# Optimization experiments

Measured on AMD Instinct MI355X. Metric: run time of the kernel, lower is better.

The kernel has to match this reference:

```python
import jax, jax.numpy as jnp
import numpy as np

NUM_EXPERTS = 8
TOP_K = 2
B, L, H = 4, 4096, 1024


def setup_inputs() -> dict:
    key = jax.random.key(0)
    ks = jax.random.split(key, 5)
    s = 1.0 / np.sqrt(H)
    return {
        "hidden_states": jax.random.normal(ks[0], (B, L, H), dtype=jnp.float32),
        "gate_w": jax.random.normal(ks[1], (H, NUM_EXPERTS), dtype=jnp.float32) * s,
        "w1": jax.random.normal(ks[2], (NUM_EXPERTS, H, 2 * H), dtype=jnp.float32) * s,
        "b1": jnp.zeros((NUM_EXPERTS, 2 * H), dtype=jnp.float32),
        "w2": jax.random.normal(ks[3], (NUM_EXPERTS, 2 * H, H), dtype=jnp.float32) * (1.0 / np.sqrt(2 * H)),
        "b2": jnp.zeros((NUM_EXPERTS, H), dtype=jnp.float32),
    }


def reference(hidden_states, gate_w, w1, b1, w2, b2):
    b, l, h = hidden_states.shape
    flat = hidden_states.reshape(-1, h)                      # [T, H]
    router_logits = flat @ gate_w                            # [T, E]
    probs = jax.nn.softmax(router_logits, axis=-1)
    weights, indices = jax.lax.top_k(probs, TOP_K)           # [T, K]
    weights = weights / jnp.sum(weights, axis=-1, keepdims=True)
    # combine[t, e] = sum_k weights[t, k] * 1{indices[t, k] == e}
    onehot = jax.nn.one_hot(indices, NUM_EXPERTS, dtype=flat.dtype)  # [T, K, E]
    combine = jnp.einsum('tk,tke->te', weights, onehot)      # [T, E]
    out = jnp.zeros_like(flat)
    for e in range(NUM_EXPERTS):  # fixed small expert loop; dense-compute, sparse-combine
        hdn = jax.nn.relu(flat @ w1[e] + b1[e])              # [T, 2H]
        y = hdn @ w2[e] + b2[e]                              # [T, H]
        out = out + combine[:, e:e + 1] * y
    return out.reshape(b, l, h)
```

## Files before the change

### kernel.cpp

```cpp
#include <hip/hip_runtime.h>
#include <hip/hip_bf16.h>
#include <stdint.h>

#define T_TOK 16384
#define HD    1024
#define HD2   2048
#define NE    8
#define ROWS  (2*T_TOK)
#define MAXT  264
#define RTOK  32

#define M_NT    256
#define M_OFFS  272
#define M_TILES 288

typedef __bf16 bf16x8 __attribute__((ext_vector_type(8)));
typedef float f32x4 __attribute__((ext_vector_type(4)));

#define GLD16(g, l) __builtin_amdgcn_global_load_lds( \
    (const __attribute__((address_space(1))) void*)(g), \
    (__attribute__((address_space(3))) void*)(l), 16, 0, 0)

__device__ inline unsigned short f2bf(float f) {
    unsigned int u = __float_as_uint(f);
    unsigned int r = (u + 0x7fffu + ((u >> 16) & 1u)) >> 16;
    return (unsigned short)r;
}

__global__ __launch_bounds__(256) void cvt_wT(const float* __restrict__ w,
                                              unsigned short* __restrict__ wt,
                                              int K, int N) {
    __shared__ float t[32][33];
    int e = blockIdx.z;
    int n0 = blockIdx.x * 32, k0 = blockIdx.y * 32;
    int r = threadIdx.x >> 3;
    int c4 = (threadIdx.x & 7) * 4;
    const float* src = w + ((size_t)e * K + k0 + r) * N + n0 + c4;
    float4 v = *(const float4*)src;
    t[r][c4] = v.x; t[r][c4+1] = v.y; t[r][c4+2] = v.z; t[r][c4+3] = v.w;
    __syncthreads();
    int cc = threadIdx.x & 7;
    ushort4 o;
    o.x = f2bf(t[cc*4+0][r]); o.y = f2bf(t[cc*4+1][r]);
    o.z = f2bf(t[cc*4+2][r]); o.w = f2bf(t[cc*4+3][r]);
    *(ushort4*)(wt + ((size_t)e * N + n0 + r) * K + k0 + cc*4) = o;
}

__global__ __launch_bounds__(256) void router_k(const float* __restrict__ x,
        const float* __restrict__ gw, int* __restrict__ meta,
        int* __restrict__ tok_e, int* __restrict__ tok_slot, float* __restrict__ tok_w,
        unsigned short* __restrict__ xb) {
    __shared__ float g[NE * HD];
    __shared__ int   le[RTOK * 2];
    __shared__ float lw[RTOK * 2];
    __shared__ int   lslot[RTOK * 2];
    __shared__ int   lcnt[NE];
    __shared__ int   lbase[NE];
    for (int i = threadIdx.x; i < NE * HD; i += 256) {
        int k = i >> 3, e = i & 7;
        g[e * HD + k] = gw[i];
    }
    if (threadIdx.x < NE) lcnt[threadIdx.x] = 0;
    __syncthreads();

    int wave = threadIdx.x >> 6, lane = threadIdx.x & 63;
    int t0 = blockIdx.x * RTOK;
    for (int i = 0; i < RTOK / 4; i++) {
        int tt = wave * (RTOK / 4) + i;
        int t = t0 + tt;
        const float4* xr = (const float4*)(x + (size_t)t * HD);
        float acc[NE];
#pragma unroll
        for (int e = 0; e < NE; e++) acc[e] = 0.f;
#pragma unroll
        for (int j = 0; j < HD / 256; j++) {
            float4 xv = xr[lane + 64 * j];
            ushort4 o4;
            o4.x = f2bf(xv.x); o4.y = f2bf(xv.y);
            o4.z = f2bf(xv.z); o4.w = f2bf(xv.w);
            *(ushort4*)(xb + (size_t)t * HD + (lane + 64 * j) * 4) = o4;
#pragma unroll
            for (int e = 0; e < NE; e++) {
                float4 gv = *(const float4*)&g[e * HD + (lane + 64 * j) * 4];
                acc[e] += xv.x * gv.x + xv.y * gv.y + xv.z * gv.z + xv.w * gv.w;
            }
        }
#pragma unroll
        for (int e = 0; e < NE; e++) {
            float v = acc[e];
#pragma unroll
            for (int off = 32; off > 0; off >>= 1) v += __shfl_down(v, off, 64);
            acc[e] = v;
        }
        if (lane == 0) {
            int e1 = 0; float l1 = acc[0];
#pragma unroll
            for (int e = 1; e < NE; e++) if (acc[e] > l1) { l1 = acc[e]; e1 = e; }
            int e2 = -1; float l2 = -3.0e38f;
#pragma unroll
            for (int e = 0; e < NE; e++) if (e != e1 && acc[e] > l2) { l2 = acc[e]; e2 = e; }
            float w1 = 1.f / (1.f + expf(l2 - l1));
            le[tt * 2] = e1;     le[tt * 2 + 1] = e2;
            lw[tt * 2] = w1;     lw[tt * 2 + 1] = 1.f - w1;
        }
    }
    __syncthreads();
    if (threadIdx.x < RTOK * 2)
        lslot[threadIdx.x] = atomicAdd(&lcnt[le[threadIdx.x]], 1);
    __syncthreads();
    if (threadIdx.x < NE)
        lbase[threadIdx.x] = atomicAdd(&meta[threadIdx.x * 32], lcnt[threadIdx.x]);
    __syncthreads();
    if (threadIdx.x < RTOK * 2) {
        int gi = t0 * 2 + threadIdx.x;
        int e = le[threadIdx.x];
        tok_e[gi]    = e;
        tok_slot[gi] = lbase[e] + lslot[threadIdx.x];
        tok_w[gi]    = lw[threadIdx.x];
    }
}

__global__ __launch_bounds__(64) void offsets_k(int* __restrict__ meta) {
    int lane = threadIdx.x;
    int cl = (lane < NE) ? meta[lane * 32] : 0;
    int cnt[NE], offs[NE], tbase[NE];
    int o = 0, tb = 0;
#pragma unroll
    for (int e = 0; e < NE; e++) {
        cnt[e] = __shfl(cl, e, 64);
        offs[e] = o;  o += cnt[e];
        tbase[e] = tb; tb += (cnt[e] + 127) >> 7;
    }
    int nt = tb;
    if (lane == 0) meta[M_NT] = nt;
    if (lane < NE) meta[M_OFFS + lane] = offs[lane];
    for (int i = lane; i < nt; i += 64) {
        int e = 0;
#pragma unroll
        for (int k = 1; k < NE; k++) if (i >= tbase[k]) e = k;
        int m = i - tbase[e];
        int r0 = offs[e] + m * 128;
        int re = offs[e] + cnt[e];
        if (r0 + 128 < re) re = r0 + 128;
        meta[M_TILES + i] = e;
        meta[M_TILES + MAXT + i] = r0;
        meta[M_TILES + 2 * MAXT + i] = re;
    }
}

__global__ __launch_bounds__(256) void scatter_k(const int* __restrict__ meta,
        const int* __restrict__ tok_e, const int* __restrict__ tok_slot,
        const float* __restrict__ tok_w, int* __restrict__ rows_tok,
        float* __restrict__ rows_w) {
    int i = blockIdx.x * 256 + threadIdx.x;
    const int* offs = meta + M_OFFS;
    int e = tok_e[i];
    int r = offs[e] + tok_slot[i];
    rows_tok[r] = i >> 1;
    rows_w[r] = tok_w[i];
}


#define ISSUE(KK, NT_) do { \
    int kk_ = (KK) < (NT_) ? (KK) : (NT_) - 1; \
    int bb_ = ((KK) & 1) * 4096; \
    GLD16(pa0 + kk_ * 32, &As[bb_ + (w * 64) * 8]); \
    GLD16(pa1 + kk_ * 32, &As[bb_ + (256 + w * 64) * 8]); \
    GLD16(pb0 + kk_ * 32, &Bs[bb_ + (w * 64) * 8]); \
    GLD16(pb1 + kk_ * 32, &Bs[bb_ + (256 + w * 64) * 8]); } while (0)
#define SB0()   __builtin_amdgcn_sched_barrier(0)
#define VMW4()  do { asm volatile("s_waitcnt vmcnt(4)" ::: "memory"); SB0(); } while (0)
#define VMW0()  do { asm volatile("s_waitcnt vmcnt(0)" ::: "memory"); SB0(); } while (0)
#define BAR()   do { __builtin_amdgcn_s_barrier(); SB0(); } while (0)
#define PRIO(P) __builtin_amdgcn_s_setprio(P)

#define KSTEP(RB) do { \
    bf16x8 af[4], bfr[4]; \
    _Pragma("unroll") \
    for (int in_ = 0; in_ < 4; in_++) { \
        int row_ = wn * 64 + in_ * 16 + rl; \
        int ph_ = q ^ ((row_ >> 1) & 3); \
        bfr[in_] = *(const bf16x8*)&Bs[(RB) + row_ * 32 + ph_ * 8]; \
    } \
    _Pragma("unroll") \
    for (int im_ = 0; im_ < 4; im_++) { \
        int row_ = wm * 64 + im_ * 16 + rl; \
        int ph_ = q ^ ((row_ >> 1) & 3); \
        af[im_] = *(const bf16x8*)&As[(RB) + row_ * 32 + ph_ * 8]; \
    } \
    _Pragma("unroll") \
    for (int im_ = 0; im_ < 4; im_++) \
    _Pragma("unroll") \
    for (int in_ = 0; in_ < 4; in_++) \
        acc[im_][in_] = __builtin_amdgcn_mfma_f32_16x16x32_bf16( \
            af[im_], bfr[in_], acc[im_][in_], 0, 0, 0); } while (0)

__global__ __launch_bounds__(256, 4) void gemm1_k(
    const unsigned short* __restrict__ Xbf,
    const unsigned short* __restrict__ W1T,
    const float* __restrict__ b1,
    const int* __restrict__ meta,
    const int* __restrict__ rows_tok,
    unsigned short* __restrict__ hdn)
{
    __shared__ unsigned short As[2 * 4096];
    __shared__ unsigned short Bs[2 * 4096];
    int nt = meta[M_NT];
    int mt = blockIdx.y;
    if (mt >= nt) return;
    int e    = meta[M_TILES + mt];
    int r0   = meta[M_TILES + MAXT + mt];
    int rend = meta[M_TILES + 2 * MAXT + mt];
    int n0 = blockIdx.x * 128;

    int tid = threadIdx.x, w = tid >> 6, lane = tid & 63;
    int wm = w & 1, wn = w >> 1;
    int rl = lane & 15, q = lane >> 4;

    const unsigned short *pa0, *pa1, *pb0, *pb1;
    {
        int gg = tid, row = gg >> 2, lc = (gg & 3) ^ ((row >> 1) & 3);
        int grow = r0 + row; grow = grow < ROWS - 1 ? grow : ROWS - 1;
        pa0 = Xbf + (size_t)rows_tok[grow] * HD + lc * 8;
        pb0 = W1T + ((size_t)e * HD2 + n0 + row) * HD + lc * 8;
        gg = 256 + tid; row = gg >> 2; lc = (gg & 3) ^ ((row >> 1) & 3);
        grow = r0 + row; grow = grow < ROWS - 1 ? grow : ROWS - 1;
        pa1 = Xbf + (size_t)rows_tok[grow] * HD + lc * 8;
        pb1 = W1T + ((size_t)e * HD2 + n0 + row) * HD + lc * 8;
    }

    f32x4 acc[4][4];
#pragma unroll
    for (int a = 0; a < 4; a++)
#pragma unroll
    for (int b = 0; b < 4; b++)
        acc[a][b] = (f32x4){0.f, 0.f, 0.f, 0.f};

    ISSUE(0, HD / 32);

#pragma unroll 2
    for (int kt = 0; kt < HD / 32; kt++) {
        ISSUE(kt + 1, HD / 32);
        SB0();
        VMW4();
        BAR();
        PRIO(1);
        KSTEP((kt & 1) * 4096);
        PRIO(0);
        BAR();
    }
    VMW0();

    const float* b1e = b1 + (size_t)e * HD2;
#pragma unroll
    for (int in = 0; in < 4; in++) {
        int col = n0 + wn * 64 + in * 16 + rl;
        float bias = b1e[col];
#pragma unroll
        for (int im = 0; im < 4; im++) {
            int rb2 = r0 + wm * 64 + im * 16 + q * 4;
#pragma unroll
            for (int j = 0; j < 4; j++) {
                int r = rb2 + j;
                if (r < rend) {
                    float v = acc[im][in][j] + bias;
                    v = v > 0.f ? v : 0.f;
                    hdn[(size_t)r * HD2 + col] = f2bf(v);
                }
            }
        }
    }
}

__global__ __launch_bounds__(256, 4) void gemm2_k(
    const unsigned short* __restrict__ hdn,
    const unsigned short* __restrict__ W2T,
    const float* __restrict__ b2,
    const int* __restrict__ meta,
    const int* __restrict__ rows_tok,
    const float* __restrict__ rows_w,
    float* __restrict__ out)
{
    __shared__ unsigned short As[2 * 4096];
    __shared__ unsigned short Bs[2 * 4096];
    int nt = meta[M_NT];
    int mt = blockIdx.y;
    if (mt >= nt) return;
    int e    = meta[M_TILES + mt];
    int r0   = meta[M_TILES + MAXT + mt];
    int rend = meta[M_TILES + 2 * MAXT + mt];
    int n0 = blockIdx.x * 128;

    int tid = threadIdx.x, w = tid >> 6, lane = tid & 63;
    int wm = w & 1, wn = w >> 1;
    int rl = lane & 15, q = lane >> 4;

    const unsigned short *pa0, *pa1, *pb0, *pb1;
    {
        int gg = tid, row = gg >> 2, lc = (gg & 3) ^ ((row >> 1) & 3);
        int grow = r0 + row; grow = grow < ROWS - 1 ? grow : ROWS - 1;
        pa0 = hdn + (size_t)grow * HD2 + lc * 8;
        pb0 = W2T + ((size_t)e * HD + n0 + row) * HD2 + lc * 8;
        gg = 256 + tid; row = gg >> 2; lc = (gg & 3) ^ ((row >> 1) & 3);
        grow = r0 + row; grow = grow < ROWS - 1 ? grow : ROWS - 1;
        pa1 = hdn + (size_t)grow * HD2 + lc * 8;
        pb1 = W2T + ((size_t)e * HD + n0 + row) * HD2 + lc * 8;
    }

    f32x4 acc[4][4];
#pragma unroll
    for (int a = 0; a < 4; a++)
#pragma unroll
    for (int b = 0; b < 4; b++)
        acc[a][b] = (f32x4){0.f, 0.f, 0.f, 0.f};

    ISSUE(0, HD2 / 32);

#pragma unroll 2
    for (int kt = 0; kt < HD2 / 32; kt++) {
        ISSUE(kt + 1, HD2 / 32);
        SB0();
        VMW4();
        BAR();
        PRIO(1);
        KSTEP((kt & 1) * 4096);
        PRIO(0);
        BAR();
    }
    VMW0();

    const float* b2e = b2 + (size_t)e * HD;
    float bias[4];
#pragma unroll
    for (int in = 0; in < 4; in++)
        bias[in] = b2e[n0 + wn * 64 + in * 16 + rl];
#pragma unroll
    for (int im = 0; im < 4; im++) {
        int rb2 = r0 + wm * 64 + im * 16 + q * 4;
#pragma unroll
        for (int j = 0; j < 4; j++) {
            int r = rb2 + j;
            if (r < rend) {
                int tok = rows_tok[r];
                float wt = rows_w[r];
                float* op = out + (size_t)tok * HD + n0 + wn * 64;
#pragma unroll
                for (int in = 0; in < 4; in++) {
                    float v = (acc[im][in][j] + bias[in]) * wt;
                    atomicAdd(op + in * 16 + rl, v);
                }
            }
        }
    }
}

extern "C" void kernel_launch(void* const* d_in, const int* in_sizes, int n_in,
                              void* d_out, int out_size, void* d_ws, size_t ws_size,
                              hipStream_t stream) {
    const float* x  = (const float*)d_in[0];
    const float* gw = (const float*)d_in[1];
    const float* w1 = (const float*)d_in[2];
    const float* b1 = (const float*)d_in[3];
    const float* w2 = (const float*)d_in[4];
    const float* b2 = (const float*)d_in[5];
    float* out = (float*)d_out;

    uint8_t* ws = (uint8_t*)d_ws;
    unsigned short* Xbf = (unsigned short*)(ws);
    unsigned short* W1T = (unsigned short*)(ws + 33554432ull);
    unsigned short* W2T = (unsigned short*)(ws + 67108864ull);
    unsigned short* HDN = (unsigned short*)(ws + 100663296ull);
    int*   meta     = (int*)(ws + 234881024ull);
    int*   tok_e    = meta + 2048;
    int*   tok_slot = tok_e + ROWS;
    float* tok_w    = (float*)(tok_slot + ROWS);
    int*   rows_tok = (int*)(tok_w + ROWS);
    float* rows_w   = (float*)(rows_tok + ROWS);

    hipMemsetAsync(meta, 0, 1024, stream);
    hipMemsetAsync(d_out, 0, (size_t)out_size * sizeof(float), stream);

    cvt_wT<<<dim3(HD2 / 32, HD / 32, NE), 256, 0, stream>>>(w1, W1T, HD, HD2);
    cvt_wT<<<dim3(HD / 32, HD2 / 32, NE), 256, 0, stream>>>(w2, W2T, HD2, HD);
    router_k<<<T_TOK / RTOK, 256, 0, stream>>>(x, gw, meta, tok_e, tok_slot, tok_w, Xbf);
    offsets_k<<<1, 64, 0, stream>>>(meta);
    scatter_k<<<ROWS / 256, 256, 0, stream>>>(meta, tok_e, tok_slot, tok_w, rows_tok, rows_w);
    gemm1_k<<<dim3(HD2 / 128, MAXT), 256, 0, stream>>>(Xbf, W1T, b1, meta, rows_tok, HDN);
    gemm2_k<<<dim3(HD / 128, MAXT), 256, 0, stream>>>(HDN, W2T, b2, meta, rows_tok, rows_w, out);
}
```

Measured before the change: 730.8 us.

## Merge weight conversions, drop offsets kernel, stage gemm1 epilogue through LDS

```diff
diff --git a/kernel.cpp b/kernel.cpp
--- a/kernel.cpp
+++ b/kernel.cpp
@@ -10,12 +10,10 @@
 #define MAXT  264
 #define RTOK  32
 
-#define M_NT    256
-#define M_OFFS  272
-#define M_TILES 288
 
 typedef __bf16 bf16x8 __attribute__((ext_vector_type(8)));
 typedef float f32x4 __attribute__((ext_vector_type(4)));
+typedef unsigned short u16x8 __attribute__((ext_vector_type(8)));
 
 #define GLD16(g, l) __builtin_amdgcn_global_load_lds( \
     (const __attribute__((address_space(1))) void*)(g), \
@@ -27,12 +25,35 @@
     return (unsigned short)r;
 }
 
-__global__ __launch_bounds__(256) void cvt_wT(const float* __restrict__ w,
-                                              unsigned short* __restrict__ wt,
-                                              int K, int N) {
+__device__ inline void tile_locate(const int* __restrict__ meta, int mt,
+                                   int* e_out, int* r0_out, int* re_out) {
+    int o = 0, tb = 0, se = -1, sr0 = 0, sre = 0;
+#pragma unroll
+    for (int k = 0; k < NE; k++) {
+        int c = meta[k * 32];
+        int t = (c + 127) >> 7;
+        if (mt >= tb && mt < tb + t) {
+            se = k;
+            sr0 = o + (mt - tb) * 128;
+            int re = o + c;
+            sre = (sr0 + 128 < re) ? sr0 + 128 : re;
+        }
+        o += c; tb += t;
+    }
+    *e_out = se; *r0_out = sr0; *re_out = sre;
+}
+
+__global__ __launch_bounds__(256) void cvt_all(const float* __restrict__ w1,
+                                               const float* __restrict__ w2,
+                                               unsigned short* __restrict__ W1T,
+                                               unsigned short* __restrict__ W2T) {
     __shared__ float t[32][33];
-    int e = blockIdx.z;
+    int z = blockIdx.z;
+    const float* w; unsigned short* wt; int K, N, e;
+    if (z < 8) { w = w1; wt = W1T; K = HD;  N = HD2; e = z; }
+    else       { w = w2; wt = W2T; K = HD2; N = HD;  e = z - 8; }
     int n0 = blockIdx.x * 32, k0 = blockIdx.y * 32;
+    if (n0 >= N || k0 >= K) return;
     int r = threadIdx.x >> 3;
     int c4 = (threadIdx.x & 7) * 4;
     const float* src = w + ((size_t)e * K + k0 + r) * N + n0 + c4;
@@ -120,42 +141,19 @@
     }
 }
 
-__global__ __launch_bounds__(64) void offsets_k(int* __restrict__ meta) {
-    int lane = threadIdx.x;
-    int cl = (lane < NE) ? meta[lane * 32] : 0;
-    int cnt[NE], offs[NE], tbase[NE];
-    int o = 0, tb = 0;
-#pragma unroll
-    for (int e = 0; e < NE; e++) {
-        cnt[e] = __shfl(cl, e, 64);
-        offs[e] = o;  o += cnt[e];
-        tbase[e] = tb; tb += (cnt[e] + 127) >> 7;
-    }
-    int nt = tb;
-    if (lane == 0) meta[M_NT] = nt;
-    if (lane < NE) meta[M_OFFS + lane] = offs[lane];
-    for (int i = lane; i < nt; i += 64) {
-        int e = 0;
-#pragma unroll
-        for (int k = 1; k < NE; k++) if (i >= tbase[k]) e = k;
-        int m = i - tbase[e];
-        int r0 = offs[e] + m * 128;
-        int re = offs[e] + cnt[e];
-        if (r0 + 128 < re) re = r0 + 128;
-        meta[M_TILES + i] = e;
-        meta[M_TILES + MAXT + i] = r0;
-        meta[M_TILES + 2 * MAXT + i] = re;
-    }
-}
-
 __global__ __launch_bounds__(256) void scatter_k(const int* __restrict__ meta,
         const int* __restrict__ tok_e, const int* __restrict__ tok_slot,
         const float* __restrict__ tok_w, int* __restrict__ rows_tok,
         float* __restrict__ rows_w) {
     int i = blockIdx.x * 256 + threadIdx.x;
-    const int* offs = meta + M_OFFS;
     int e = tok_e[i];
-    int r = offs[e] + tok_slot[i];
+    int off = 0;
+#pragma unroll
+    for (int k = 0; k < NE; k++) {
+        int c = meta[k * 32];
+        off += (k < e) ? c : 0;
+    }
+    int r = off + tok_slot[i];
     rows_tok[r] = i >> 1;
     rows_w[r] = tok_w[i];
 }
@@ -205,12 +203,9 @@
 {
     __shared__ unsigned short As[2 * 4096];
     __shared__ unsigned short Bs[2 * 4096];
-    int nt = meta[M_NT];
-    int mt = blockIdx.y;
-    if (mt >= nt) return;
-    int e    = meta[M_TILES + mt];
-    int r0   = meta[M_TILES + MAXT + mt];
-    int rend = meta[M_TILES + 2 * MAXT + mt];
+    int e, r0, rend;
+    tile_locate(meta, blockIdx.y, &e, &r0, &rend);
+    if (e < 0) return;
     int n0 = blockIdx.x * 128;
 
     int tid = threadIdx.x, w = tid >> 6, lane = tid & 63;
@@ -250,25 +245,40 @@
         BAR();
     }
     VMW0();
-
-    const float* b1e = b1 + (size_t)e * HD2;
-#pragma unroll
-    for (int in = 0; in < 4; in++) {
-        int col = n0 + wn * 64 + in * 16 + rl;
-        float bias = b1e[col];
-#pragma unroll
-        for (int im = 0; im < 4; im++) {
-            int rb2 = r0 + wm * 64 + im * 16 + q * 4;
-#pragma unroll
-            for (int j = 0; j < 4; j++) {
-                int r = rb2 + j;
-                if (r < rend) {
+    BAR();
+
+    {
+        const float* b1e = b1 + (size_t)e * HD2;
+        unsigned short* obuf = wn ? (unsigned short*)Bs : (unsigned short*)As;
+#pragma unroll
+        for (int in = 0; in < 4; in++) {
+            int ci = in * 16 + rl;
+            float bias = b1e[n0 + wn * 64 + ci];
+#pragma unroll
+            for (int im = 0; im < 4; im++) {
+                int rowb = wm * 64 + im * 16 + q * 4;
+#pragma unroll
+                for (int j = 0; j < 4; j++) {
+                    int row = rowb + j;
                     float v = acc[im][in][j] + bias;
                     v = v > 0.f ? v : 0.f;
-                    hdn[(size_t)r * HD2 + col] = f2bf(v);
+                    int gc = ci >> 3;
+                    obuf[row * 64 + (((gc ^ (row & 7)) << 3) | (ci & 7))] = f2bf(v);
                 }
             }
         }
+    }
+    BAR();
+#pragma unroll
+    for (int it = 0; it < 8; it++) {
+        int row = it * 16 + (tid >> 4);
+        int gran = tid & 15;
+        const unsigned short* ibuf = (gran < 8) ? (const unsigned short*)As
+                                                : (const unsigned short*)Bs;
+        u16x8 v = *(const u16x8*)&ibuf[row * 64 + (((gran & 7) ^ (row & 7)) << 3)];
+        int r = r0 + row;
+        if (r < rend)
+            *(u16x8*)&hdn[(size_t)r * HD2 + n0 + gran * 8] = v;
     }
 }
 
@@ -283,12 +293,9 @@
 {
     __shared__ unsigned short As[2 * 4096];
     __shared__ unsigned short Bs[2 * 4096];
-    int nt = meta[M_NT];
-    int mt = blockIdx.y;
-    if (mt >= nt) return;
-    int e    = meta[M_TILES + mt];
-    int r0   = meta[M_TILES + MAXT + mt];
-    int rend = meta[M_TILES + 2 * MAXT + mt];
+    int e, r0, rend;
+    tile_locate(meta, blockIdx.y, &e, &r0, &rend);
+    if (e < 0) return;
     int n0 = blockIdx.x * 128;
 
     int tid = threadIdx.x, w = tid >> 6, lane = tid & 63;
@@ -380,10 +387,8 @@
     hipMemsetAsync(meta, 0, 1024, stream);
     hipMemsetAsync(d_out, 0, (size_t)out_size * sizeof(float), stream);
 
-    cvt_wT<<<dim3(HD2 / 32, HD / 32, NE), 256, 0, stream>>>(w1, W1T, HD, HD2);
-    cvt_wT<<<dim3(HD / 32, HD2 / 32, NE), 256, 0, stream>>>(w2, W2T, HD2, HD);
+    cvt_all<<<dim3(64, 64, 16), 256, 0, stream>>>(w1, w2, W1T, W2T);
     router_k<<<T_TOK / RTOK, 256, 0, stream>>>(x, gw, meta, tok_e, tok_slot, tok_w, Xbf);
-    offsets_k<<<1, 64, 0, stream>>>(meta);
     scatter_k<<<ROWS / 256, 256, 0, stream>>>(meta, tok_e, tok_slot, tok_w, rows_tok, rows_w);
     gemm1_k<<<dim3(HD2 / 128, MAXT), 256, 0, stream>>>(Xbf, W1T, b1, meta, rows_tok, HDN);
     gemm2_k<<<dim3(HD / 128, MAXT), 256, 0, stream>>>(HDN, W2T, b2, meta, rows_tok, rows_w, out);
```

After: 680.5 us. -6.9%, faster.
